# Kernel tuning notes

Hardware: AMD Instinct MI355X
Metric: run time of the kernel (lower is better)

Reference implementation:

```python
import jax, jax.numpy as jnp
import numpy as np

N = 100000   # nodes
E = 800000   # edges
IN = 64      # in_channels
H = 128      # hidden_channels (Embedding_Dimension)
K = 9        # Num_TCN clusters
EPS = 1e-15


def setup_inputs() -> dict:
    key = jax.random.key(0)
    k0, k1, k2, k3, k4 = jax.random.split(key, 5)
    x = jax.random.normal(k0, (N, IN), jnp.float32)
    edge_index = jax.random.randint(k1, (2, E), 0, N, dtype=jnp.int32)
    batch = jnp.zeros((N,), jnp.int32)  # single graph
    W1 = jax.random.normal(k2, (IN, H), jnp.float32) / np.sqrt(IN)
    b1 = jnp.zeros((H,), jnp.float32)
    Wp = jax.random.normal(k3, (H, K), jnp.float32) / np.sqrt(H)
    bp = jax.random.normal(k4, (K,), jnp.float32) * 0.01
    return {"x": x, "edge_index": edge_index, "batch": batch,
            "W1": W1, "b1": b1, "Wp": Wp, "bp": bp}


def gcn_conv(x, edge_index, W, b):
    # GCNConv: h = D^{-1/2} (A + I) D^{-1/2} (x W) + b
    n = x.shape[0]
    h = x @ W  # [N, H]
    loop = jnp.arange(n, dtype=edge_index.dtype)
    row = jnp.concatenate([edge_index[0], loop])  # source
    col = jnp.concatenate([edge_index[1], loop])  # target
    deg = jax.ops.segment_sum(jnp.ones_like(col, jnp.float32), col, n)
    dinv = jax.lax.rsqrt(jnp.maximum(deg, 1.0))  # deg >= 1 (self loops)
    norm = dinv[row] * dinv[col]  # [E+N]
    agg = jax.ops.segment_sum(norm[:, None] * h[row], col, n)  # scatter-add at targets
    return agg + b


def reference(x, edge_index, batch, W1, b1, Wp, bp):
    n = x.shape[0]
    src, dst = edge_index[0], edge_index[1]

    hx = jax.nn.relu(gcn_conv(x, edge_index, W1, b1))  # [N, H]
    s_logits = hx @ Wp + bp                             # [N, K]
    s = jax.nn.softmax(s_logits, axis=-1)

    # pooled features and adjacency: S^T X, S^T A S (A sparse via edge list)
    x_pool = s.T @ hx                                   # [K, H]
    out_adj = jnp.einsum('ek,el->kl', s[src], s[dst])   # [K, K]

    # mincut loss: -Tr(S^T A S) / Tr(S^T D S)
    mincut_num = jnp.trace(out_adj)
    deg_a = jax.ops.segment_sum(jnp.ones((src.shape[0],), jnp.float32), dst, n)
    mincut_den = jnp.sum(deg_a * jnp.sum(s * s, axis=-1))
    mc = -(mincut_num / (mincut_den + EPS))

    # orthogonality loss: || S^T S / ||S^T S||_F - I/sqrt(K) ||_F
    ss = s.T @ s
    o = jnp.linalg.norm(ss / jnp.linalg.norm(ss) - jnp.eye(K, dtype=s.dtype) / jnp.sqrt(jnp.float32(K)))

    # normalize pooled adjacency: zero diag, symmetric degree normalization
    oa = out_adj * (1.0 - jnp.eye(K, dtype=out_adj.dtype))
    d = jnp.sum(oa, axis=-1)
    dis = jax.lax.rsqrt(d + EPS)
    oa = dis[:, None] * oa * dis[None, :]

    out = jax.nn.log_softmax(x_pool[None], axis=-1)     # [1, K, H]
    return out, mc, o, s, oa[None]
```

## Files before the change

### kernel.cpp

```cpp
#include <hip/hip_runtime.h>
#include <hip/hip_bf16.h>

#define NN 100000
#define NE 800000
#define INC 64
#define HID 128
#define KC 9
#define NBKT 782
#define BCAP 2048

#define G_XP 0
#define G_OA 1152
#define G_SS 1233
#define G_DEN 1314

__device__ __forceinline__ float atomAddG(float* p, float v) {
  return unsafeAtomicAdd(p, v);
}


__global__ __launch_bounds__(256) void k_binA(const int* __restrict__ src, const int* __restrict__ dst,
                                              int* __restrict__ bcur, int* __restrict__ ebuf) {
  __shared__ int hist[NBKT];
  __shared__ int hbase[NBKT];
  int t = threadIdx.x;
  for (int b = t; b < NBKT; b += 256) hist[b] = 0;
  __syncthreads();
  int beg = blockIdx.x * 6250, end = beg + 6250;
  for (int i = beg + t; i < end; i += 256) atomicAdd(&hist[dst[i] >> 7], 1);
  __syncthreads();
  for (int b = t; b < NBKT; b += 256) {
    int h = hist[b];
    hbase[b] = h ? atomicAdd(&bcur[b], h) : 0;
    hist[b] = 0;
  }
  __syncthreads();
  for (int i = beg + t; i < end; i += 256) {
    int d = dst[i], s = src[i];
    int b = d >> 7;
    int r = atomicAdd(&hist[b], 1);
    ebuf[(size_t)b * BCAP + hbase[b] + r] = s | ((d & 127) << 17);
  }
}

__global__ __launch_bounds__(256) void k_scanb(const int* __restrict__ bcur, int* __restrict__ bbase) {
  __shared__ int sc[1024];
  int t = threadIdx.x;
  for (int i = t; i < 1024; i += 256) sc[i] = (i < NBKT) ? bcur[i] : 0;
  __syncthreads();
  for (int off = 1; off < 1024; off <<= 1) {
    int v0 = (t >= off) ? sc[t - off] : 0;
    int v1 = (t + 256 >= off) ? sc[t + 256 - off] : 0;
    int v2 = (t + 512 >= off) ? sc[t + 512 - off] : 0;
    int v3 = (t + 768 >= off) ? sc[t + 768 - off] : 0;
    __syncthreads();
    sc[t] += v0; sc[t + 256] += v1; sc[t + 512] += v2; sc[t + 768] += v3;
    __syncthreads();
  }
  for (int i = t; i < NBKT; i += 256) bbase[i] = sc[i] - bcur[i];
}

__global__ __launch_bounds__(256) void k_fillB(const int* __restrict__ bcur, const int* __restrict__ bbase,
                                               const int* __restrict__ ebuf, int* __restrict__ rowptr,
                                               int* __restrict__ degi, float* __restrict__ dinv,
                                               int* __restrict__ csr) {
  __shared__ int cnt[128], loc[128], lcur[128];
  int b = blockIdx.x;
  int t = threadIdx.x;
  if (t < 128) cnt[t] = 0;
  __syncthreads();
  int n = bcur[b];
  const int* eb = ebuf + (size_t)b * BCAP;
  for (int i = t; i < n; i += 256) atomicAdd(&cnt[eb[i] >> 17], 1);
  __syncthreads();
  if (t < 128) loc[t] = cnt[t];
  __syncthreads();
  for (int off = 1; off < 128; off <<= 1) {
    int u = (t >= off && t < 128) ? loc[t - off] : 0;
    __syncthreads();
    if (t < 128) loc[t] += u;
    __syncthreads();
  }
  int gbase = bbase[b];
  if (t < 128) {
    int node = (b << 7) + t;
    int rp = gbase + loc[t] - cnt[t];
    if (node < NN) {
      rowptr[node] = rp;
      degi[node] = cnt[t];
      dinv[node] = rsqrtf((float)cnt[t] + 1.f);
    }
    lcur[t] = rp;
  }
  __syncthreads();
  for (int i = t; i < n; i += 256) {
    int pack = eb[i];
    int s = pack & 0x1FFFF;
    int dl = pack >> 17;
    int p = atomicAdd(&lcur[dl], 1);
    csr[p] = s;
  }
}


__global__ __launch_bounds__(256) void k_gather(const int* __restrict__ rowptr, const int* __restrict__ degi,
                                                const int* __restrict__ csr, const float* __restrict__ x,
                                                const float* __restrict__ dinv, float* __restrict__ agg) {
  int t = threadIdx.x;
  int wave = t >> 6, lane = t & 63;
  int gw = blockIdx.x * 4 + wave;
  int ng = lane >> 4, c4 = lane & 15;
  int node = gw * 4 + ng;
  if (node >= NN) return;

  float dv = dinv[node];
  int base = rowptr[node];
  int cnt = degi[node];

  float4 xs = ((const float4*)(x + (size_t)node * INC))[c4];
  float dv2 = dv * dv;
  float4 acc;
  acc.x = dv2 * xs.x; acc.y = dv2 * xs.y; acc.z = dv2 * xs.z; acc.w = dv2 * xs.w;

  int j = 0;
  for (; j + 3 < cnt; j += 4) {
    int s0 = csr[base + j], s1 = csr[base + j + 1], s2 = csr[base + j + 2], s3 = csr[base + j + 3];
    float w0 = dinv[s0] * dv, w1 = dinv[s1] * dv, w2 = dinv[s2] * dv, w3 = dinv[s3] * dv;
    float4 r0 = ((const float4*)(x + (size_t)s0 * INC))[c4];
    float4 r1 = ((const float4*)(x + (size_t)s1 * INC))[c4];
    float4 r2 = ((const float4*)(x + (size_t)s2 * INC))[c4];
    float4 r3 = ((const float4*)(x + (size_t)s3 * INC))[c4];
    acc.x = fmaf(w0, r0.x, acc.x); acc.y = fmaf(w0, r0.y, acc.y);
    acc.z = fmaf(w0, r0.z, acc.z); acc.w = fmaf(w0, r0.w, acc.w);
    acc.x = fmaf(w1, r1.x, acc.x); acc.y = fmaf(w1, r1.y, acc.y);
    acc.z = fmaf(w1, r1.z, acc.z); acc.w = fmaf(w1, r1.w, acc.w);
    acc.x = fmaf(w2, r2.x, acc.x); acc.y = fmaf(w2, r2.y, acc.y);
    acc.z = fmaf(w2, r2.z, acc.z); acc.w = fmaf(w2, r2.w, acc.w);
    acc.x = fmaf(w3, r3.x, acc.x); acc.y = fmaf(w3, r3.y, acc.y);
    acc.z = fmaf(w3, r3.z, acc.z); acc.w = fmaf(w3, r3.w, acc.w);
  }
  for (; j < cnt; ++j) {
    int si = csr[base + j];
    float w = dinv[si] * dv;
    float4 r = ((const float4*)(x + (size_t)si * INC))[c4];
    acc.x = fmaf(w, r.x, acc.x); acc.y = fmaf(w, r.y, acc.y);
    acc.z = fmaf(w, r.z, acc.z); acc.w = fmaf(w, r.w, acc.w);
  }
  ((float4*)(agg + (size_t)node * INC))[c4] = acc;
}


__global__ __launch_bounds__(256, 2) void k_mlpA(const float* __restrict__ agg,
                                                 const float* __restrict__ W1, const float* __restrict__ b1,
                                                 const float* __restrict__ Wp, const float* __restrict__ bp,
                                                 float* __restrict__ s_out, float* __restrict__ s_pad,
                                                 float* __restrict__ h_glob) {
  __shared__ float W1s[INC * HID];
  __shared__ float Wps[HID * 12];
  __shared__ float b1s[HID];

  int t = threadIdx.x;
  for (int i = t; i < (INC * HID) / 4; i += 256) ((float4*)W1s)[i] = ((const float4*)W1)[i];
  for (int i = t; i < HID * KC; i += 256) { int c = i / KC, q = i - c * KC; Wps[c * 12 + q] = Wp[i]; }
  if (t < HID) b1s[t] = b1[t];
  __syncthreads();

  int node = blockIdx.x * 256 + t;
  if (node >= NN) return;

  float a[INC];
  {
    const float4* arow = (const float4*)(agg + (size_t)node * INC);
#pragma unroll
    for (int i = 0; i < 16; ++i) {
      float4 v = arow[i];
      a[4 * i + 0] = v.x; a[4 * i + 1] = v.y; a[4 * i + 2] = v.z; a[4 * i + 3] = v.w;
    }
  }

  float logit[KC];
#pragma unroll
  for (int q = 0; q < KC; ++q) logit[q] = bp[q];

  float4* hout = (float4*)(h_glob + (size_t)node * HID);

#pragma unroll 1
  for (int ch = 0; ch < 8; ++ch) {
    float h16[16];
    {
      const float4* bv = (const float4*)&b1s[ch * 16];
#pragma unroll
      for (int i = 0; i < 4; ++i) {
        float4 v = bv[i];
        h16[4 * i + 0] = v.x; h16[4 * i + 1] = v.y; h16[4 * i + 2] = v.z; h16[4 * i + 3] = v.w;
      }
    }
#pragma unroll
    for (int k = 0; k < INC; ++k) {
      const float4* wrow = (const float4*)&W1s[k * HID + ch * 16];
      float ak = a[k];
#pragma unroll
      for (int i = 0; i < 4; ++i) {
        float4 w = wrow[i];
        h16[4 * i + 0] = fmaf(ak, w.x, h16[4 * i + 0]);
        h16[4 * i + 1] = fmaf(ak, w.y, h16[4 * i + 1]);
        h16[4 * i + 2] = fmaf(ak, w.z, h16[4 * i + 2]);
        h16[4 * i + 3] = fmaf(ak, w.w, h16[4 * i + 3]);
      }
    }
#pragma unroll
    for (int i = 0; i < 16; ++i) {
      float hr = fmaxf(h16[i], 0.f);
      h16[i] = hr;
      const float4* wp = (const float4*)&Wps[(ch * 16 + i) * 12];
      float4 w0 = wp[0], w1 = wp[1], w2 = wp[2];
      logit[0] = fmaf(hr, w0.x, logit[0]);
      logit[1] = fmaf(hr, w0.y, logit[1]);
      logit[2] = fmaf(hr, w0.z, logit[2]);
      logit[3] = fmaf(hr, w0.w, logit[3]);
      logit[4] = fmaf(hr, w1.x, logit[4]);
      logit[5] = fmaf(hr, w1.y, logit[5]);
      logit[6] = fmaf(hr, w1.z, logit[6]);
      logit[7] = fmaf(hr, w1.w, logit[7]);
      logit[8] = fmaf(hr, w2.x, logit[8]);
    }
#pragma unroll
    for (int i = 0; i < 4; ++i)
      hout[ch * 4 + i] = make_float4(h16[4 * i], h16[4 * i + 1], h16[4 * i + 2], h16[4 * i + 3]);
  }

  float m = logit[0];
#pragma unroll
  for (int q = 1; q < KC; ++q) m = fmaxf(m, logit[q]);
  float Z = 0.f;
#pragma unroll
  for (int q = 0; q < KC; ++q) { logit[q] = __expf(logit[q] - m); Z += logit[q]; }
  float inv = 1.0f / Z;
#pragma unroll
  for (int q = 0; q < KC; ++q) logit[q] *= inv;

  float* so = s_out + (size_t)node * KC;
#pragma unroll
  for (int q = 0; q < KC; ++q) so[q] = logit[q];
  float4* sp = (float4*)(s_pad + (size_t)node * 12);
  sp[0] = make_float4(logit[0], logit[1], logit[2], logit[3]);
  sp[1] = make_float4(logit[4], logit[5], logit[6], logit[7]);
  sp[2] = make_float4(logit[8], 0.f, 0.f, 0.f);
}


__global__ __launch_bounds__(256) void k_poolB(const float* __restrict__ h_glob,
                                               const float* __restrict__ s_pad,
                                               const int* __restrict__ degi,
                                               float* __restrict__ glob) {
  int t = threadIdx.x;
  int wave = t >> 6, lane = t & 63;
  int gw = blockIdx.x * 4 + wave;
  int nw = gridDim.x * 4;
  const int c0 = 2 * lane;

  float pool0[KC], pool1[KC], ssr[KC];
  float den_acc = 0.f;
#pragma unroll
  for (int q = 0; q < KC; ++q) { pool0[q] = 0.f; pool1[q] = 0.f; ssr[q] = 0.f; }

  for (int node0 = gw; node0 < NN; node0 += nw) {
    int node = __builtin_amdgcn_readfirstlane(node0);
    float2 hv = *(const float2*)&h_glob[(size_t)node * HID + c0];
    const float* srow = s_pad + (size_t)node * 12;
    float4 s0 = *(const float4*)srow;
    float4 s1 = *(const float4*)(srow + 4);
    float s8 = srow[8];
    float sb[KC] = {s0.x, s0.y, s0.z, s0.w, s1.x, s1.y, s1.z, s1.w, s8};
    float sq = (lane < KC) ? srow[lane] : 0.f;
    float dg = (float)degi[node];

#pragma unroll
    for (int q = 0; q < KC; ++q) {
      pool0[q] = fmaf(sb[q], hv.x, pool0[q]);
      pool1[q] = fmaf(sb[q], hv.y, pool1[q]);
    }
    if (lane < KC) {
#pragma unroll
      for (int q = 0; q < KC; ++q) ssr[q] = fmaf(sq, sb[q], ssr[q]);
      den_acc = fmaf(dg * sq, sq, den_acc);
    }
  }

  __shared__ float pool_sh[KC * HID + 82];
  float* ss_sh = pool_sh + KC * HID;
  float* den_sh = ss_sh + 81;
  for (int i = t; i < KC * HID + 82; i += 256) pool_sh[i] = 0.f;
  __syncthreads();

#pragma unroll
  for (int q = 0; q < KC; ++q) {
    atomicAdd(&pool_sh[q * HID + c0], pool0[q]);
    atomicAdd(&pool_sh[q * HID + c0 + 1], pool1[q]);
  }
  if (lane < KC) {
#pragma unroll
    for (int q = 0; q < KC; ++q) atomicAdd(&ss_sh[lane * KC + q], ssr[q]);
    atomicAdd(den_sh, den_acc);
  }
  __syncthreads();

  for (int i = t; i < KC * HID; i += 256) atomAddG(&glob[G_XP + i], pool_sh[i]);
  if (t < KC * KC) atomAddG(&glob[G_SS + t], ss_sh[t]);
  if (t == 0) atomAddG(&glob[G_DEN], *den_sh);
}


__global__ __launch_bounds__(256) void k_adj(const int* __restrict__ rowptr, const int* __restrict__ degi,
                                             const int* __restrict__ csr, const float* __restrict__ s_pad,
                                             float* __restrict__ oa_g) {
  int t = threadIdx.x;
  int tid = blockIdx.x * blockDim.x + t;
  int stride = gridDim.x * blockDim.x;

  float acc[81];
#pragma unroll
  for (int i = 0; i < 81; ++i) acc[i] = 0.f;

  for (int node = tid; node < NN; node += stride) {
    int base = rowptr[node];
    int cnt = degi[node];
    float4 g0 = make_float4(0.f, 0.f, 0.f, 0.f);
    float4 g1 = g0;
    float g8 = 0.f;
    int j = 0;
    for (; j + 1 < cnt; j += 2) {
      int s0 = csr[base + j], s1 = csr[base + j + 1];
      const float4* p0 = (const float4*)(s_pad + (size_t)s0 * 12);
      const float4* p1 = (const float4*)(s_pad + (size_t)s1 * 12);
      float4 a0 = p0[0], b0 = p0[1], c0 = p0[2];
      float4 a1 = p1[0], b1 = p1[1], c1 = p1[2];
      g0.x += a0.x + a1.x; g0.y += a0.y + a1.y; g0.z += a0.z + a1.z; g0.w += a0.w + a1.w;
      g1.x += b0.x + b1.x; g1.y += b0.y + b1.y; g1.z += b0.z + b1.z; g1.w += b0.w + b1.w;
      g8 += c0.x + c1.x;
    }
    if (j < cnt) {
      int s0 = csr[base + j];
      const float4* p0 = (const float4*)(s_pad + (size_t)s0 * 12);
      float4 a0 = p0[0], b0 = p0[1], c0 = p0[2];
      g0.x += a0.x; g0.y += a0.y; g0.z += a0.z; g0.w += a0.w;
      g1.x += b0.x; g1.y += b0.y; g1.z += b0.z; g1.w += b0.w;
      g8 += c0.x;
    }
    const float4* sn = (const float4*)(s_pad + (size_t)node * 12);
    float4 d0 = sn[0], d1 = sn[1], d2 = sn[2];
    float gg[9] = {g0.x, g0.y, g0.z, g0.w, g1.x, g1.y, g1.z, g1.w, g8};
    float sd[9] = {d0.x, d0.y, d0.z, d0.w, d1.x, d1.y, d1.z, d1.w, d2.x};
#pragma unroll
    for (int i = 0; i < 9; ++i)
#pragma unroll
      for (int jj = 0; jj < 9; ++jj) acc[i * 9 + jj] = fmaf(gg[i], sd[jj], acc[i * 9 + jj]);
  }

  __shared__ float wsum[4][81];
#pragma unroll
  for (int i = 0; i < 81; ++i) {
#pragma unroll
    for (int off = 32; off > 0; off >>= 1) acc[i] += __shfl_xor(acc[i], off, 64);
  }
  int wave = t >> 6, lane = t & 63;
  if (lane == 0) {
#pragma unroll
    for (int i = 0; i < 81; ++i) wsum[wave][i] = acc[i];
  }
  __syncthreads();
  if (t < 81) atomAddG(&oa_g[t], wsum[0][t] + wsum[1][t] + wsum[2][t] + wsum[3][t]);
}


__global__ __launch_bounds__(128) void k_final(const float* __restrict__ glob, float* __restrict__ out) {
  const float* xp = glob + G_XP;
  const float* oa = glob + G_OA;
  const float* ssm = glob + G_SS;
  const float* den = glob + G_DEN;
  int t = threadIdx.x;
  __shared__ float red[128];

  for (int k = 0; k < 9; ++k) {
    float v = xp[k * 128 + t];
    red[t] = v;
    __syncthreads();
    for (int s2 = 64; s2 > 0; s2 >>= 1) {
      if (t < s2) red[t] = fmaxf(red[t], red[t + s2]);
      __syncthreads();
    }
    float m = red[0];
    __syncthreads();
    red[t] = expf(v - m);
    __syncthreads();
    for (int s2 = 64; s2 > 0; s2 >>= 1) {
      if (t < s2) red[t] += red[t + s2];
      __syncthreads();
    }
    float lz = logf(red[0]) + m;
    __syncthreads();
    out[k * 128 + t] = v - lz;
  }

  if (t == 0) {
    float num = 0.f;
    for (int q = 0; q < 9; ++q) num += oa[q * 9 + q];
    out[1152] = -(num / (den[0] + 1e-15f));

    float fn = 0.f;
    for (int i = 0; i < 81; ++i) fn += ssm[i] * ssm[i];
    float rfn = 1.0f / sqrtf(fn);
    float osum = 0.f;
    for (int i = 0; i < 9; ++i)
      for (int j = 0; j < 9; ++j) {
        float v = ssm[i * 9 + j] * rfn - ((i == j) ? (1.0f / 3.0f) : 0.f);
        osum += v * v;
      }
    out[1153] = sqrtf(osum);
  }

  __shared__ float dsh[9];
  if (t < 9) {
    float d = 0.f;
    for (int j = 0; j < 9; ++j)
      if (j != t) d += oa[t * 9 + j];
    dsh[t] = 1.0f / sqrtf(d + 1e-15f);
  }
  __syncthreads();
  if (t < 81) {
    int i = t / 9, j = t % 9;
    out[901154 + t] = (i == j) ? 0.f : dsh[i] * oa[t] * dsh[j];
  }
}

extern "C" void kernel_launch(void* const* d_in, const int* in_sizes, int n_in,
                              void* d_out, int out_size, void* d_ws, size_t ws_size,
                              hipStream_t stream) {
  const float* x = (const float*)d_in[0];
  const int* ei = (const int*)d_in[1];
  const float* W1 = (const float*)d_in[3];
  const float* b1 = (const float*)d_in[4];
  const float* Wp = (const float*)d_in[5];
  const float* bp = (const float*)d_in[6];
  float* out = (float*)d_out;

  float* glob = (float*)d_ws;
  int* bcur = (int*)d_ws + 1316;
  int* bbase = (int*)d_ws + 2116;
  int* rowptr = (int*)d_ws + 2944;
  int* degi = rowptr + NN;
  int* csr = degi + NN;
  float* dinv = (float*)(csr + NE);
  float* s_pad = dinv + NN;
  float* agg = s_pad + (size_t)NN * 12;
  float* h_glob = agg + (size_t)NN * INC;
  int* ebuf = (int*)h_glob;

  hipMemsetAsync(d_ws, 0, (size_t)2116 * sizeof(float), stream);

  const int* src = ei;
  const int* dst = ei + NE;

  hipLaunchKernelGGL(k_binA, dim3(128), dim3(256), 0, stream, src, dst, bcur, ebuf);
  hipLaunchKernelGGL(k_scanb, dim3(1), dim3(256), 0, stream, bcur, bbase);
  hipLaunchKernelGGL(k_fillB, dim3(NBKT), dim3(256), 0, stream, bcur, bbase, ebuf,
                     rowptr, degi, dinv, csr);
  hipLaunchKernelGGL(k_gather, dim3(6250), dim3(256), 0, stream, rowptr, degi, csr, x, dinv, agg);
  hipLaunchKernelGGL(k_mlpA, dim3((NN + 255) / 256), dim3(256), 0, stream, agg,
                     W1, b1, Wp, bp, out + 1154, s_pad, h_glob);
  hipLaunchKernelGGL(k_poolB, dim3(512), dim3(256), 0, stream, h_glob, s_pad, degi, glob);
  hipLaunchKernelGGL(k_adj, dim3(1024), dim3(256), 0, stream, rowptr, degi, csr, s_pad, glob + G_OA);
  hipLaunchKernelGGL(k_final, dim3(1), dim3(128), 0, stream, glob, out);
}
```

Before: 295.0 us.

## Compute GCN hidden layer with split-bf16 MFMA instead of scalar FMA

Rewrites the dense 64x128 projection in the MLP kernel to use bf16 MFMA instructions, with each fp32 operand split into hi and lo bf16 parts and three products summed to keep close to fp32 accuracy. Each block now handles 128 nodes staged in LDS, and the small Wp projection is done per lane followed by a 16-lane shuffle reduction. The aim is to move the dominant FLOPs off the vector ALU. In exchange it adds conversion work, extra LDS traffic, strided h_glob stores and shuffle reductions, and it carries a small precision risk.

After: 301.7 us. 2.3% more time.

```diff
diff --git a/kernel.cpp b/kernel.cpp
--- a/kernel.cpp
+++ b/kernel.cpp
@@ -8,14 +8,23 @@
 #define KC 9
 #define NBKT 782
 #define BCAP 2048
+#define LDA 72
 
 #define G_XP 0
 #define G_OA 1152
 #define G_SS 1233
 #define G_DEN 1314
 
+typedef __attribute__((ext_vector_type(8))) short bfrag;
+typedef __attribute__((ext_vector_type(4))) float facc4;
+
 __device__ __forceinline__ float atomAddG(float* p, float v) {
   return unsafeAtomicAdd(p, v);
+}
+
+__device__ __forceinline__ unsigned short bf16rn(float x) {
+  unsigned u = __float_as_uint(x);
+  return (unsigned short)((u + 0x7fffu + ((u >> 16) & 1u)) >> 16);
 }
 
 
@@ -155,97 +164,149 @@
                                                  const float* __restrict__ Wp, const float* __restrict__ bp,
                                                  float* __restrict__ s_out, float* __restrict__ s_pad,
                                                  float* __restrict__ h_glob) {
-  __shared__ float W1s[INC * HID];
-  __shared__ float Wps[HID * 12];
-  __shared__ float b1s[HID];
-
-  int t = threadIdx.x;
-  for (int i = t; i < (INC * HID) / 4; i += 256) ((float4*)W1s)[i] = ((const float4*)W1)[i];
-  for (int i = t; i < HID * KC; i += 256) { int c = i / KC, q = i - c * KC; Wps[c * 12 + q] = Wp[i]; }
-  if (t < HID) b1s[t] = b1[t];
-  __syncthreads();
-
-  int node = blockIdx.x * 256 + t;
-  if (node >= NN) return;
-
-  float a[INC];
-  {
-    const float4* arow = (const float4*)(agg + (size_t)node * INC);
-#pragma unroll
-    for (int i = 0; i < 16; ++i) {
-      float4 v = arow[i];
-      a[4 * i + 0] = v.x; a[4 * i + 1] = v.y; a[4 * i + 2] = v.z; a[4 * i + 3] = v.w;
-    }
-  }
-
-  float logit[KC];
-#pragma unroll
-  for (int q = 0; q < KC; ++q) logit[q] = bp[q];
-
-  float4* hout = (float4*)(h_glob + (size_t)node * HID);
+  __shared__ short Ahi[128 * LDA];
+  __shared__ short Alo[128 * LDA];
+  __shared__ short Whi[128 * LDA];
+  __shared__ short Wlo[128 * LDA];
+
+  int t = threadIdx.x;
+  int nbase = blockIdx.x * 128;
+
+#pragma unroll
+  for (int j = 0; j < 8; ++j) {
+    int task = t + 256 * j;
+    int n = task >> 4, kq = (task & 15) * 4;
+    float4 v = make_float4(0.f, 0.f, 0.f, 0.f);
+    if (nbase + n < NN) v = *(const float4*)(agg + (size_t)(nbase + n) * INC + kq);
+    unsigned short h0 = bf16rn(v.x), h1 = bf16rn(v.y), h2 = bf16rn(v.z), h3 = bf16rn(v.w);
+    float l0f = v.x - __uint_as_float((unsigned)h0 << 16);
+    float l1f = v.y - __uint_as_float((unsigned)h1 << 16);
+    float l2f = v.z - __uint_as_float((unsigned)h2 << 16);
+    float l3f = v.w - __uint_as_float((unsigned)h3 << 16);
+    unsigned short q0 = bf16rn(l0f), q1 = bf16rn(l1f), q2 = bf16rn(l2f), q3 = bf16rn(l3f);
+    *(uint2*)&Ahi[n * LDA + kq] = make_uint2((unsigned)h0 | ((unsigned)h1 << 16),
+                                             (unsigned)h2 | ((unsigned)h3 << 16));
+    *(uint2*)&Alo[n * LDA + kq] = make_uint2((unsigned)q0 | ((unsigned)q1 << 16),
+                                             (unsigned)q2 | ((unsigned)q3 << 16));
+  }
+#pragma unroll
+  for (int j = 0; j < 8; ++j) {
+    int task = t + 256 * j;
+    int c = task & 127, kq = (task >> 7) * 4;
+    float v0 = W1[(kq + 0) * HID + c];
+    float v1 = W1[(kq + 1) * HID + c];
+    float v2 = W1[(kq + 2) * HID + c];
+    float v3 = W1[(kq + 3) * HID + c];
+    unsigned short h0 = bf16rn(v0), h1 = bf16rn(v1), h2 = bf16rn(v2), h3 = bf16rn(v3);
+    float l0f = v0 - __uint_as_float((unsigned)h0 << 16);
+    float l1f = v1 - __uint_as_float((unsigned)h1 << 16);
+    float l2f = v2 - __uint_as_float((unsigned)h2 << 16);
+    float l3f = v3 - __uint_as_float((unsigned)h3 << 16);
+    unsigned short q0 = bf16rn(l0f), q1 = bf16rn(l1f), q2 = bf16rn(l2f), q3 = bf16rn(l3f);
+    *(uint2*)&Whi[c * LDA + kq] = make_uint2((unsigned)h0 | ((unsigned)h1 << 16),
+                                             (unsigned)h2 | ((unsigned)h3 << 16));
+    *(uint2*)&Wlo[c * LDA + kq] = make_uint2((unsigned)q0 | ((unsigned)q1 << 16),
+                                             (unsigned)q2 | ((unsigned)q3 << 16));
+  }
+  __syncthreads();
+
+  int w = t >> 6, l = t & 63;
+  int r0 = w * 32;
+  int lrow = l & 15;
+  int lk = (l >> 4) * 8;
+  int rg = (l >> 4) * 4;
+
+  facc4 acc[2][8];
+#pragma unroll
+  for (int mt = 0; mt < 2; ++mt)
+#pragma unroll
+    for (int nt = 0; nt < 8; ++nt) acc[mt][nt] = (facc4){0.f, 0.f, 0.f, 0.f};
+
+#pragma unroll
+  for (int ks = 0; ks < 2; ++ks) {
+    int ko = ks * 32 + lk;
+    bfrag a0h = *(const bfrag*)&Ahi[(r0 + lrow) * LDA + ko];
+    bfrag a0l = *(const bfrag*)&Alo[(r0 + lrow) * LDA + ko];
+    bfrag a1h = *(const bfrag*)&Ahi[(r0 + 16 + lrow) * LDA + ko];
+    bfrag a1l = *(const bfrag*)&Alo[(r0 + 16 + lrow) * LDA + ko];
+#pragma unroll
+    for (int nt = 0; nt < 8; ++nt) {
+      bfrag bh = *(const bfrag*)&Whi[(nt * 16 + lrow) * LDA + ko];
+      bfrag bl = *(const bfrag*)&Wlo[(nt * 16 + lrow) * LDA + ko];
+      acc[0][nt] = __builtin_amdgcn_mfma_f32_16x16x32_bf16(a0l, bh, acc[0][nt], 0, 0, 0);
+      acc[0][nt] = __builtin_amdgcn_mfma_f32_16x16x32_bf16(a0h, bl, acc[0][nt], 0, 0, 0);
+      acc[0][nt] = __builtin_amdgcn_mfma_f32_16x16x32_bf16(a0h, bh, acc[0][nt], 0, 0, 0);
+      acc[1][nt] = __builtin_amdgcn_mfma_f32_16x16x32_bf16(a1l, bh, acc[1][nt], 0, 0, 0);
+      acc[1][nt] = __builtin_amdgcn_mfma_f32_16x16x32_bf16(a1h, bl, acc[1][nt], 0, 0, 0);
+      acc[1][nt] = __builtin_amdgcn_mfma_f32_16x16x32_bf16(a1h, bh, acc[1][nt], 0, 0, 0);
+    }
+  }
+
+  float plg[2][4][KC];
+#pragma unroll
+  for (int mt = 0; mt < 2; ++mt)
+#pragma unroll
+    for (int r = 0; r < 4; ++r)
+#pragma unroll
+      for (int q = 0; q < KC; ++q) plg[mt][r][q] = 0.f;
 
 #pragma unroll 1
-  for (int ch = 0; ch < 8; ++ch) {
-    float h16[16];
-    {
-      const float4* bv = (const float4*)&b1s[ch * 16];
-#pragma unroll
-      for (int i = 0; i < 4; ++i) {
-        float4 v = bv[i];
-        h16[4 * i + 0] = v.x; h16[4 * i + 1] = v.y; h16[4 * i + 2] = v.z; h16[4 * i + 3] = v.w;
+  for (int nt = 0; nt < 8; ++nt) {
+    int c = nt * 16 + lrow;
+    float b1v = b1[c];
+    float wp[KC];
+#pragma unroll
+    for (int q = 0; q < KC; ++q) wp[q] = Wp[c * KC + q];
+#pragma unroll
+    for (int mt = 0; mt < 2; ++mt) {
+      int nodeb = nbase + r0 + mt * 16 + rg;
+#pragma unroll
+      for (int r = 0; r < 4; ++r) {
+        float h = fmaxf(acc[mt][nt][r] + b1v, 0.f);
+        if (nodeb + r < NN) h_glob[(size_t)(nodeb + r) * HID + c] = h;
+#pragma unroll
+        for (int q = 0; q < KC; ++q) plg[mt][r][q] = fmaf(h, wp[q], plg[mt][r][q]);
       }
     }
-#pragma unroll
-    for (int k = 0; k < INC; ++k) {
-      const float4* wrow = (const float4*)&W1s[k * HID + ch * 16];
-      float ak = a[k];
-#pragma unroll
-      for (int i = 0; i < 4; ++i) {
-        float4 w = wrow[i];
-        h16[4 * i + 0] = fmaf(ak, w.x, h16[4 * i + 0]);
-        h16[4 * i + 1] = fmaf(ak, w.y, h16[4 * i + 1]);
-        h16[4 * i + 2] = fmaf(ak, w.z, h16[4 * i + 2]);
-        h16[4 * i + 3] = fmaf(ak, w.w, h16[4 * i + 3]);
-      }
-    }
-#pragma unroll
-    for (int i = 0; i < 16; ++i) {
-      float hr = fmaxf(h16[i], 0.f);
-      h16[i] = hr;
-      const float4* wp = (const float4*)&Wps[(ch * 16 + i) * 12];
-      float4 w0 = wp[0], w1 = wp[1], w2 = wp[2];
-      logit[0] = fmaf(hr, w0.x, logit[0]);
-      logit[1] = fmaf(hr, w0.y, logit[1]);
-      logit[2] = fmaf(hr, w0.z, logit[2]);
-      logit[3] = fmaf(hr, w0.w, logit[3]);
-      logit[4] = fmaf(hr, w1.x, logit[4]);
-      logit[5] = fmaf(hr, w1.y, logit[5]);
-      logit[6] = fmaf(hr, w1.z, logit[6]);
-      logit[7] = fmaf(hr, w1.w, logit[7]);
-      logit[8] = fmaf(hr, w2.x, logit[8]);
-    }
-#pragma unroll
-    for (int i = 0; i < 4; ++i)
-      hout[ch * 4 + i] = make_float4(h16[4 * i], h16[4 * i + 1], h16[4 * i + 2], h16[4 * i + 3]);
-  }
-
-  float m = logit[0];
-#pragma unroll
-  for (int q = 1; q < KC; ++q) m = fmaxf(m, logit[q]);
-  float Z = 0.f;
-#pragma unroll
-  for (int q = 0; q < KC; ++q) { logit[q] = __expf(logit[q] - m); Z += logit[q]; }
-  float inv = 1.0f / Z;
-#pragma unroll
-  for (int q = 0; q < KC; ++q) logit[q] *= inv;
-
-  float* so = s_out + (size_t)node * KC;
-#pragma unroll
-  for (int q = 0; q < KC; ++q) so[q] = logit[q];
-  float4* sp = (float4*)(s_pad + (size_t)node * 12);
-  sp[0] = make_float4(logit[0], logit[1], logit[2], logit[3]);
-  sp[1] = make_float4(logit[4], logit[5], logit[6], logit[7]);
-  sp[2] = make_float4(logit[8], 0.f, 0.f, 0.f);
+  }
+
+#pragma unroll
+  for (int off = 1; off < 16; off <<= 1) {
+#pragma unroll
+    for (int mt = 0; mt < 2; ++mt)
+#pragma unroll
+      for (int r = 0; r < 4; ++r)
+#pragma unroll
+        for (int q = 0; q < KC; ++q)
+          plg[mt][r][q] += __shfl_xor(plg[mt][r][q], off, 16);
+  }
+
+  float bpv[KC];
+#pragma unroll
+  for (int q = 0; q < KC; ++q) bpv[q] = bp[q];
+  int j = lrow;
+#pragma unroll
+  for (int mt = 0; mt < 2; ++mt) {
+#pragma unroll
+    for (int r = 0; r < 4; ++r) {
+      int node = nbase + r0 + mt * 16 + rg + r;
+      if (node >= NN) continue;
+      float lg[KC];
+#pragma unroll
+      for (int q = 0; q < KC; ++q) lg[q] = plg[mt][r][q] + bpv[q];
+      float m = lg[0];
+#pragma unroll
+      for (int q = 1; q < KC; ++q) m = fmaxf(m, lg[q]);
+      float Z = 0.f;
+#pragma unroll
+      for (int q = 0; q < KC; ++q) { lg[q] = __expf(lg[q] - m); Z += lg[q]; }
+      float inv = 1.0f / Z;
+#pragma unroll
+      for (int q = 0; q < KC; ++q) lg[q] *= inv;
+      if (j < KC) s_out[(size_t)node * KC + j] = lg[j];
+      if (j < 12) s_pad[(size_t)node * 12 + j] = (j < KC) ? lg[j] : 0.f;
+    }
+  }
 }
 
 
@@ -466,7 +527,7 @@
   hipLaunchKernelGGL(k_fillB, dim3(NBKT), dim3(256), 0, stream, bcur, bbase, ebuf,
                      rowptr, degi, dinv, csr);
   hipLaunchKernelGGL(k_gather, dim3(6250), dim3(256), 0, stream, rowptr, degi, csr, x, dinv, agg);
-  hipLaunchKernelGGL(k_mlpA, dim3((NN + 255) / 256), dim3(256), 0, stream, agg,
+  hipLaunchKernelGGL(k_mlpA, dim3(NBKT), dim3(256), 0, stream, agg,
                      W1, b1, Wp, bp, out + 1154, s_pad, h_glob);
   hipLaunchKernelGGL(k_poolB, dim3(512), dim3(256), 0, stream, h_glob, s_pad, degi, glob);
   hipLaunchKernelGGL(k_adj, dim3(1024), dim3(256), 0, stream, rowptr, degi, csr, s_pad, glob + G_OA);
```
